# Performance work log

Hardware: AMD Instinct MI355X
Metric: run time of the kernel (lower is better)

Reference implementation:

```python
import jax, jax.numpy as jnp
import numpy as np

N_SRC0, N_DST0, N_DST1 = 100000, 25000, 5000
E0, E1 = 800000, 160000
D = 256


def setup_inputs() -> dict:
    key = jax.random.key(0)
    k = jax.random.split(key, 7)
    return {
        "x": jax.random.normal(k[0], (N_SRC0, D), dtype=jnp.float32),
        "ew0": jax.random.uniform(k[1], (E0,), dtype=jnp.float32),
        "ew1": jax.random.uniform(k[2], (E1,), dtype=jnp.float32),
        "src0": jax.random.randint(k[3], (E0,), 0, N_SRC0, dtype=jnp.int32),
        "dst0": jax.random.randint(k[4], (E0,), 0, N_DST0, dtype=jnp.int32),
        "src1": jax.random.randint(k[5], (E1,), 0, N_DST0, dtype=jnp.int32),
        "dst1": jax.random.randint(k[6], (E1,), 0, N_DST1, dtype=jnp.int32),
    }


def _block(x, src, dst, ew, n_dst):
    # u_mul_e + sum: gather src features, scale by edge weight, scatter-sum to dst
    msgs = x[src] * ew[:, None]            # [E, D]
    return jax.ops.segment_sum(msgs, dst, num_segments=n_dst)  # [n_dst, D]


def reference(x, ew0, ew1, src0, dst0, src1, dst1):
    h = _block(x, src0, dst0, ew0, N_DST0)   # block 0: [N_DST0, D]
    h = _block(h, src1, dst1, ew1, N_DST1)   # block 1: [N_DST1, D]
    return h
```

## Files before the change

### kernel.cpp

```cpp
#include <hip/hip_runtime.h>

constexpr int D       = 256;
constexpr int DV4     = D / 4;
constexpr int N_DST0  = 25000;
constexpr int N_DST1  = 5000;
constexpr int NARENA  = 8;
constexpr int CAPX    = 24;


__device__ __forceinline__ unsigned pack_bf16(float a, float b) {
    unsigned ua = __float_as_uint(a);
    unsigned ub = __float_as_uint(b);
    ua = (ua + 0x7FFFu + ((ua >> 16) & 1u)) >> 16;
    ub = (ub + 0x7FFFu + ((ub >> 16) & 1u)) >> 16;
    return ua | (ub << 16);
}

__device__ __forceinline__ void fma8_bf16(float* acc, uint4 v, float w) {
    acc[0] += __uint_as_float(v.x << 16)          * w;
    acc[1] += __uint_as_float(v.x & 0xFFFF0000u)  * w;
    acc[2] += __uint_as_float(v.y << 16)          * w;
    acc[3] += __uint_as_float(v.y & 0xFFFF0000u)  * w;
    acc[4] += __uint_as_float(v.z << 16)          * w;
    acc[5] += __uint_as_float(v.z & 0xFFFF0000u)  * w;
    acc[6] += __uint_as_float(v.w << 16)          * w;
    acc[7] += __uint_as_float(v.w & 0xFFFF0000u)  * w;
}

__device__ __forceinline__ unsigned pack_edge(int s, float w) {
    unsigned wq = (unsigned)(w * 32768.0f + 0.5f);
    wq = min(wq, 32767u);
    return (unsigned)s | (wq << 17);
}


__global__ __launch_bounds__(256) void prep_fused(
    const float4* __restrict__ x4, uint2* __restrict__ xb, int n4, int Gc,
    const int* __restrict__ src0, const float* __restrict__ ew0,
    const int* __restrict__ dst0, int E0, int* __restrict__ cnt0,
    unsigned* __restrict__ meta0,
    const int* __restrict__ src1, const float* __restrict__ ew1,
    const int* __restrict__ dst1, int E1, int* __restrict__ cnt1,
    unsigned* __restrict__ meta1)
{
    if (blockIdx.x < Gc) {
        int i = blockIdx.x * blockDim.x + threadIdx.x;
        int stride = Gc * blockDim.x;
        for (; i < n4; i += stride) {
            float4 v = x4[i];
            xb[i] = make_uint2(pack_bf16(v.x, v.y), pack_bf16(v.z, v.w));
        }
    } else {
        int arena = blockIdx.x & (NARENA - 1);
        int i = (blockIdx.x - Gc) * blockDim.x + threadIdx.x;
        int stride = (gridDim.x - Gc) * blockDim.x;
        int total = E0 + E1;
        for (; i < total; i += stride) {
            if (i < E0) {
                int s = src0[i];
                float w = ew0[i];
                int d = dst0[i];
                int p = atomicAdd(&cnt0[arena * N_DST0 + d], 1);
                if (p < CAPX)
                    meta0[((size_t)arena * N_DST0 + d) * CAPX + p] = pack_edge(s, w);
            } else {
                int q = i - E0;
                int s = src1[q];
                float w = ew1[q];
                int d = dst1[q];
                int p = atomicAdd(&cnt1[arena * N_DST1 + d], 1);
                if (p < CAPX)
                    meta1[((size_t)arena * N_DST1 + d) * CAPX + p] = pack_edge(s, w);
            }
        }
    }
}


template <bool OUT_BF16>
__global__ __launch_bounds__(256) void gather_cap(
    const uint4* __restrict__ xb4,
    const uint*  __restrict__ meta,
    const int*   __restrict__ cnt,
    void*        __restrict__ outp,
    int n_dst)
{
    int wave = (int)((blockIdx.x * blockDim.x + threadIdx.x) >> 6);
    int lane = threadIdx.x & 63;
    if (wave >= n_dst) return;

    int half = lane >> 5;
    int c16  = lane & 31;

    int cx = (lane < NARENA) ? min(cnt[lane * n_dst + wave], CAPX) : 0;
    int o[NARENA + 1];
    o[0] = 0;
    #pragma unroll
    for (int x = 0; x < NARENA; ++x) o[x + 1] = o[x] + __shfl(cx, x, 64);
    int n = o[NARENA];

    float acc[8] = {0.f,0.f,0.f,0.f,0.f,0.f,0.f,0.f};

    for (int base = 0; base < n; base += 64) {
        int i = base + lane;
        int2 mm = make_int2(0, 0);
        if (i < n) {
            int x = 0;
            #pragma unroll
            for (int y = 1; y < NARENA; ++y) if (i >= o[y]) x = y;
            unsigned u = meta[((size_t)x * n_dst + wave) * CAPX + (i - o[x])];
            mm.x = (int)(u & 0x1FFFFu);
            mm.y = __float_as_int((float)(u >> 17) * (1.0f / 32768.0f));
        }
        int nk = min(64, n - base);

        for (int e = 0; e < nk; e += 8) {
            int   sA = __shfl(mm.x, e + 0 + half, 64);
            int   sB = __shfl(mm.x, e + 2 + half, 64);
            int   sC = __shfl(mm.x, e + 4 + half, 64);
            int   sD = __shfl(mm.x, e + 6 + half, 64);
            float wA = __int_as_float(__shfl(mm.y, e + 0 + half, 64));
            float wB = __int_as_float(__shfl(mm.y, e + 2 + half, 64));
            float wC = __int_as_float(__shfl(mm.y, e + 4 + half, 64));
            float wD = __int_as_float(__shfl(mm.y, e + 6 + half, 64));
            uint4 vA = xb4[(size_t)sA * 32 + c16];
            uint4 vB = xb4[(size_t)sB * 32 + c16];
            uint4 vC = xb4[(size_t)sC * 32 + c16];
            uint4 vD = xb4[(size_t)sD * 32 + c16];
            fma8_bf16(acc, vA, wA);
            fma8_bf16(acc, vB, wB);
            fma8_bf16(acc, vC, wC);
            fma8_bf16(acc, vD, wD);
        }
    }

    #pragma unroll
    for (int j = 0; j < 8; ++j) acc[j] += __shfl_xor(acc[j], 32, 64);

    if (half == 0) {
        if (OUT_BF16) {
            uint4 o4;
            o4.x = pack_bf16(acc[0], acc[1]);
            o4.y = pack_bf16(acc[2], acc[3]);
            o4.z = pack_bf16(acc[4], acc[5]);
            o4.w = pack_bf16(acc[6], acc[7]);
            ((uint4*)outp)[(size_t)wave * 32 + c16] = o4;
        } else {
            float4* of = (float4*)outp;
            of[(size_t)wave * 64 + c16 * 2 + 0] = make_float4(acc[0], acc[1], acc[2], acc[3]);
            of[(size_t)wave * 64 + c16 * 2 + 1] = make_float4(acc[4], acc[5], acc[6], acc[7]);
        }
    }
}


__global__ __launch_bounds__(256) void hist_both(
    const int* __restrict__ dst0, int E0, int* __restrict__ cnt0,
    const int* __restrict__ dst1, int E1, int* __restrict__ cnt1)
{
    int i = blockIdx.x * blockDim.x + threadIdx.x;
    int stride = gridDim.x * blockDim.x;
    int total = E0 + E1;
    for (; i < total; i += stride) {
        if (i < E0) atomicAdd(&cnt0[dst0[i]], 1);
        else        atomicAdd(&cnt1[dst1[i - E0]], 1);
    }
}

__device__ void scan_one(int* cnt, int* row, int n)
{
    const int T = 1024;
    int t   = threadIdx.x;
    int per = (n + T - 1) / T;
    int b   = t * per;
    int e   = min(b + per, n);

    int local = 0;
    for (int i = b; i < e; ++i) local += cnt[i];

    int lane = t & 63, wid = t >> 6;
    int v = local;
    #pragma unroll
    for (int off = 1; off < 64; off <<= 1) {
        int u = __shfl_up(v, off, 64);
        if (lane >= off) v += u;
    }

    __shared__ int wsum[16], woff[16];
    if (lane == 63) wsum[wid] = v;
    __syncthreads();
    if (t == 0) {
        int run = 0;
        #pragma unroll
        for (int i = 0; i < 16; ++i) { woff[i] = run; run += wsum[i]; }
        row[n] = run;
    }
    __syncthreads();

    int run = woff[wid] + (v - local);
    for (int i = b; i < e; ++i) {
        int c = cnt[i];
        row[i] = run;
        cnt[i] = run;
        run += c;
    }
}

__global__ __launch_bounds__(1024) void scan_both(
    int* cnt0, int* row0, int n0, int* cnt1, int* row1, int n1)
{
    if (blockIdx.x == 0) scan_one(cnt0, row0, n0);
    else                 scan_one(cnt1, row1, n1);
}

__global__ __launch_bounds__(256) void scatter_both(
    const int* __restrict__ src0, const float* __restrict__ ew0,
    const int* __restrict__ dst0, int E0, int* __restrict__ cur0,
    int2* __restrict__ meta0,
    const int* __restrict__ src1, const float* __restrict__ ew1,
    const int* __restrict__ dst1, int E1, int* __restrict__ cur1,
    int2* __restrict__ meta1)
{
    int i = blockIdx.x * blockDim.x + threadIdx.x;
    int stride = gridDim.x * blockDim.x;
    int total = E0 + E1;
    for (; i < total; i += stride) {
        if (i < E0) {
            int p = atomicAdd(&cur0[dst0[i]], 1);
            meta0[p] = make_int2(src0[i], __float_as_int(ew0[i]));
        } else {
            int j = i - E0;
            int p = atomicAdd(&cur1[dst1[j]], 1);
            meta1[p] = make_int2(src1[j], __float_as_int(ew1[j]));
        }
    }
}

__global__ __launch_bounds__(256) void gather_rows_f32(
    const float* __restrict__ xin,
    const int2*  __restrict__ meta,
    const int*   __restrict__ row_start,
    float*       __restrict__ outp,
    int n_dst)
{
    int wave = (int)((blockIdx.x * blockDim.x + threadIdx.x) >> 6);
    int lane = threadIdx.x & 63;
    if (wave >= n_dst) return;

    int beg = row_start[wave];
    int end = row_start[wave + 1];
    const float4* xv = reinterpret_cast<const float4*>(xin);

    float4 acc = {0.f, 0.f, 0.f, 0.f};
    for (int base = beg; base < end; base += 64) {
        int idx = base + lane;
        int2 m = (idx < end) ? meta[idx] : make_int2(0, 0);
        int nk = min(64, end - base);
        int k = 0;
        for (; k + 4 <= nk; k += 4) {
            float4 v0 = xv[(size_t)__shfl(m.x, k + 0, 64) * DV4 + lane];
            float4 v1 = xv[(size_t)__shfl(m.x, k + 1, 64) * DV4 + lane];
            float4 v2 = xv[(size_t)__shfl(m.x, k + 2, 64) * DV4 + lane];
            float4 v3 = xv[(size_t)__shfl(m.x, k + 3, 64) * DV4 + lane];
            float w0 = __int_as_float(__shfl(m.y, k + 0, 64));
            float w1 = __int_as_float(__shfl(m.y, k + 1, 64));
            float w2 = __int_as_float(__shfl(m.y, k + 2, 64));
            float w3 = __int_as_float(__shfl(m.y, k + 3, 64));
            acc.x += v0.x * w0; acc.y += v0.y * w0; acc.z += v0.z * w0; acc.w += v0.w * w0;
            acc.x += v1.x * w1; acc.y += v1.y * w1; acc.z += v1.z * w1; acc.w += v1.w * w1;
            acc.x += v2.x * w2; acc.y += v2.y * w2; acc.z += v2.z * w2; acc.w += v2.w * w2;
            acc.x += v3.x * w3; acc.y += v3.y * w3; acc.z += v3.z * w3; acc.w += v3.w * w3;
        }
        for (; k < nk; ++k) {
            float4 v = xv[(size_t)__shfl(m.x, k, 64) * DV4 + lane];
            float w  = __int_as_float(__shfl(m.y, k, 64));
            acc.x += v.x * w; acc.y += v.y * w; acc.z += v.z * w; acc.w += v.w * w;
        }
    }
    reinterpret_cast<float4*>(outp)[(size_t)wave * DV4 + lane] = acc;
}


extern "C" void kernel_launch(void* const* d_in, const int* in_sizes, int n_in,
                              void* d_out, int out_size, void* d_ws, size_t ws_size,
                              hipStream_t stream) {
    const float* x    = (const float*)d_in[0];
    const float* ew0  = (const float*)d_in[1];
    const float* ew1  = (const float*)d_in[2];
    const int*   src0 = (const int*)d_in[3];
    const int*   dst0 = (const int*)d_in[4];
    const int*   src1 = (const int*)d_in[5];
    const int*   dst1 = (const int*)d_in[6];
    float*       out  = (float*)d_out;

    const int E0    = in_sizes[1];
    const int E1    = in_sizes[2];
    const int N_SRC = in_sizes[0] / D;

    const int blk = 256;
    int g0 = (N_DST0 * 64 + blk - 1) / blk;
    int g1 = (N_DST1 * 64 + blk - 1) / blk;
    int n4 = N_SRC * D / 4;

    size_t need_t1 =
        (size_t)N_SRC * D * 2 +
        (size_t)N_DST0 * D * 2 +
        (size_t)NARENA * N_DST0 * CAPX * 4 +
        (size_t)NARENA * N_DST1 * CAPX * 4 +
        (size_t)NARENA * (N_DST0 + N_DST1) * 4 +
        1024;

    if (ws_size >= need_t1) {
        char* p = (char*)d_ws;
        uint2* xb    = (uint2*)p;    p += (size_t)N_SRC * D * 2;
        uint2* h0b   = (uint2*)p;    p += (size_t)N_DST0 * D * 2;
        unsigned* meta0 = (unsigned*)p; p += (size_t)NARENA * N_DST0 * CAPX * 4;
        unsigned* meta1 = (unsigned*)p; p += (size_t)NARENA * N_DST1 * CAPX * 4;
        int*   cnt0  = (int*)p;      p += (size_t)NARENA * N_DST0 * 4;
        int*   cnt1  = (int*)p;      p += (size_t)NARENA * N_DST1 * 4;

        hipMemsetAsync(cnt0, 0, (size_t)NARENA * (N_DST0 + N_DST1) * 4, stream);

        const int Gc = 1024, Gs = 2048;
        prep_fused<<<Gc + Gs, blk, 0, stream>>>(
            (const float4*)x, xb, n4, Gc,
            src0, ew0, dst0, E0, cnt0, meta0,
            src1, ew1, dst1, E1, cnt1, meta1);

        gather_cap<true ><<<g0, blk, 0, stream>>>(
            (const uint4*)xb,  meta0, cnt0, (void*)h0b, N_DST0);
        gather_cap<false><<<g1, blk, 0, stream>>>(
            (const uint4*)h0b, meta1, cnt1, (void*)out, N_DST1);
    } else {
        char* p = (char*)d_ws;
        float* h0    = (float*)p; p += (size_t)N_DST0 * D * sizeof(float);
        int2*  meta0 = (int2*)p;  p += (size_t)E0 * sizeof(int2);
        int2*  meta1 = (int2*)p;  p += (size_t)E1 * sizeof(int2);
        int*   cnt0  = (int*)p;   p += (size_t)N_DST0 * sizeof(int);
        int*   row0  = (int*)p;   p += (size_t)(N_DST0 + 1) * sizeof(int);
        int*   cnt1  = (int*)p;   p += (size_t)N_DST1 * sizeof(int);
        int*   row1  = (int*)p;   p += (size_t)(N_DST1 + 1) * sizeof(int);

        hipMemsetAsync(cnt0, 0, (size_t)N_DST0 * sizeof(int), stream);
        hipMemsetAsync(cnt1, 0, (size_t)N_DST1 * sizeof(int), stream);

        int gEdges = min((E0 + E1 + blk - 1) / blk, 3840);
        hist_both<<<gEdges, blk, 0, stream>>>(dst0, E0, cnt0, dst1, E1, cnt1);
        scan_both<<<2, 1024, 0, stream>>>(cnt0, row0, N_DST0, cnt1, row1, N_DST1);
        scatter_both<<<gEdges, blk, 0, stream>>>(src0, ew0, dst0, E0, cnt0, meta0,
                                                 src1, ew1, dst1, E1, cnt1, meta1);
        gather_rows_f32<<<g0, blk, 0, stream>>>(x,  meta0, row0, h0,  N_DST0);
        gather_rows_f32<<<g1, blk, 0, stream>>>(h0, meta1, row1, out, N_DST1);
    }
}
```

Before: 140.5 us.

## Move block-1 edge scatter into block-0 gather kernel and rebalance prep grid

Block-1 edge bucketing no longer runs in the prep kernel. It now happens in dedicated blocks of the block-0 gather launch, so it overlaps with the block-0 gather. The prep kernel handles only the bf16 conversion and block-0 scatter, with its block split changed to 1280 convert and 768 scatter blocks. The fallback path's edge grid cap is also reduced. This shortens the critical prep phase, but the extra scatter blocks compete with the bandwidth-heavy gather for resources.

```diff
diff --git a/kernel.cpp b/kernel.cpp
--- a/kernel.cpp
+++ b/kernel.cpp
@@ -34,61 +34,31 @@
 }
 
 
-__global__ __launch_bounds__(256) void prep_fused(
-    const float4* __restrict__ x4, uint2* __restrict__ xb, int n4, int Gc,
-    const int* __restrict__ src0, const float* __restrict__ ew0,
-    const int* __restrict__ dst0, int E0, int* __restrict__ cnt0,
-    unsigned* __restrict__ meta0,
-    const int* __restrict__ src1, const float* __restrict__ ew1,
-    const int* __restrict__ dst1, int E1, int* __restrict__ cnt1,
-    unsigned* __restrict__ meta1)
-{
-    if (blockIdx.x < Gc) {
-        int i = blockIdx.x * blockDim.x + threadIdx.x;
-        int stride = Gc * blockDim.x;
-        for (; i < n4; i += stride) {
-            float4 v = x4[i];
-            xb[i] = make_uint2(pack_bf16(v.x, v.y), pack_bf16(v.z, v.w));
-        }
-    } else {
-        int arena = blockIdx.x & (NARENA - 1);
-        int i = (blockIdx.x - Gc) * blockDim.x + threadIdx.x;
-        int stride = (gridDim.x - Gc) * blockDim.x;
-        int total = E0 + E1;
-        for (; i < total; i += stride) {
-            if (i < E0) {
-                int s = src0[i];
-                float w = ew0[i];
-                int d = dst0[i];
-                int p = atomicAdd(&cnt0[arena * N_DST0 + d], 1);
-                if (p < CAPX)
-                    meta0[((size_t)arena * N_DST0 + d) * CAPX + p] = pack_edge(s, w);
-            } else {
-                int q = i - E0;
-                int s = src1[q];
-                float w = ew1[q];
-                int d = dst1[q];
-                int p = atomicAdd(&cnt1[arena * N_DST1 + d], 1);
-                if (p < CAPX)
-                    meta1[((size_t)arena * N_DST1 + d) * CAPX + p] = pack_edge(s, w);
-            }
-        }
+__device__ __forceinline__ void scatter_edges(
+    const int* __restrict__ src, const float* __restrict__ ew,
+    const int* __restrict__ dst, int E,
+    int* __restrict__ cnt, unsigned* __restrict__ meta, int n_dst,
+    int arena, int i0, int stride)
+{
+    for (int i = i0; i < E; i += stride) {
+        int s = src[i];
+        float w = ew[i];
+        int d = dst[i];
+        int p = atomicAdd(&cnt[arena * n_dst + d], 1);
+        if (p < CAPX)
+            meta[((size_t)arena * n_dst + d) * CAPX + p] = pack_edge(s, w);
     }
 }
 
 
 template <bool OUT_BF16>
-__global__ __launch_bounds__(256) void gather_cap(
+__device__ __forceinline__ void gather_row(
     const uint4* __restrict__ xb4,
-    const uint*  __restrict__ meta,
-    const int*   __restrict__ cnt,
-    void*        __restrict__ outp,
-    int n_dst)
-{
-    int wave = (int)((blockIdx.x * blockDim.x + threadIdx.x) >> 6);
-    int lane = threadIdx.x & 63;
-    if (wave >= n_dst) return;
-
+    const unsigned* __restrict__ meta,
+    const int* __restrict__ cnt,
+    void* __restrict__ outp,
+    int n_dst, int wave, int lane)
+{
     int half = lane >> 5;
     int c16  = lane & 31;
 
@@ -151,6 +121,62 @@
             of[(size_t)wave * 64 + c16 * 2 + 1] = make_float4(acc[4], acc[5], acc[6], acc[7]);
         }
     }
+}
+
+
+__global__ __launch_bounds__(256) void prep0(
+    const float4* __restrict__ x4, uint2* __restrict__ xb, int n4, int Gc,
+    const int* __restrict__ src0, const float* __restrict__ ew0,
+    const int* __restrict__ dst0, int E0,
+    int* __restrict__ cnt0, unsigned* __restrict__ meta0)
+{
+    if (blockIdx.x < Gc) {
+        int i = blockIdx.x * blockDim.x + threadIdx.x;
+        int stride = Gc * blockDim.x;
+        for (; i < n4; i += stride) {
+            float4 v = x4[i];
+            xb[i] = make_uint2(pack_bf16(v.x, v.y), pack_bf16(v.z, v.w));
+        }
+    } else {
+        int arena = blockIdx.x & (NARENA - 1);
+        int i0 = (blockIdx.x - Gc) * blockDim.x + threadIdx.x;
+        int stride = (gridDim.x - Gc) * blockDim.x;
+        scatter_edges(src0, ew0, dst0, E0, cnt0, meta0, N_DST0, arena, i0, stride);
+    }
+}
+
+
+__global__ __launch_bounds__(256) void gather0_scatter1(
+    const uint4* __restrict__ xb4,
+    const unsigned* __restrict__ meta0, const int* __restrict__ cnt0,
+    uint2* __restrict__ h0b,
+    const int* __restrict__ src1, const float* __restrict__ ew1,
+    const int* __restrict__ dst1, int E1,
+    int* __restrict__ cnt1, unsigned* __restrict__ meta1, int S1B)
+{
+    if ((int)blockIdx.x < S1B) {
+        int arena = blockIdx.x & (NARENA - 1);
+        int i0 = blockIdx.x * blockDim.x + threadIdx.x;
+        int stride = S1B * blockDim.x;
+        scatter_edges(src1, ew1, dst1, E1, cnt1, meta1, N_DST1, arena, i0, stride);
+        return;
+    }
+    int wave = (int)((((int)blockIdx.x - S1B) * blockDim.x + threadIdx.x) >> 6);
+    int lane = threadIdx.x & 63;
+    if (wave < N_DST0)
+        gather_row<true>(xb4, meta0, cnt0, (void*)h0b, N_DST0, wave, lane);
+}
+
+
+__global__ __launch_bounds__(256) void gather1_k(
+    const uint4* __restrict__ h0b4,
+    const unsigned* __restrict__ meta1, const int* __restrict__ cnt1,
+    float* __restrict__ outp)
+{
+    int wave = (int)((blockIdx.x * blockDim.x + threadIdx.x) >> 6);
+    int lane = threadIdx.x & 63;
+    if (wave < N_DST1)
+        gather_row<false>(h0b4, meta1, cnt1, (void*)outp, N_DST1, wave, lane);
 }
 
 
@@ -298,8 +324,6 @@
     const int N_SRC = in_sizes[0] / D;
 
     const int blk = 256;
-    int g0 = (N_DST0 * 64 + blk - 1) / blk;
-    int g1 = (N_DST1 * 64 + blk - 1) / blk;
     int n4 = N_SRC * D / 4;
 
     size_t need_t1 =
@@ -321,16 +345,20 @@
 
         hipMemsetAsync(cnt0, 0, (size_t)NARENA * (N_DST0 + N_DST1) * 4, stream);
 
-        const int Gc = 1024, Gs = 2048;
-        prep_fused<<<Gc + Gs, blk, 0, stream>>>(
+        const int Gc = 1280, Gs = 768;
+        prep0<<<Gc + Gs, blk, 0, stream>>>(
             (const float4*)x, xb, n4, Gc,
-            src0, ew0, dst0, E0, cnt0, meta0,
-            src1, ew1, dst1, E1, cnt1, meta1);
-
-        gather_cap<true ><<<g0, blk, 0, stream>>>(
-            (const uint4*)xb,  meta0, cnt0, (void*)h0b, N_DST0);
-        gather_cap<false><<<g1, blk, 0, stream>>>(
-            (const uint4*)h0b, meta1, cnt1, (void*)out, N_DST1);
+            src0, ew0, dst0, E0, cnt0, meta0);
+
+        const int S1B = 512;
+        int g0 = S1B + (N_DST0 * 64 + blk - 1) / blk;
+        gather0_scatter1<<<g0, blk, 0, stream>>>(
+            (const uint4*)xb, meta0, cnt0, h0b,
+            src1, ew1, dst1, E1, cnt1, meta1, S1B);
+
+        int g1 = (N_DST1 * 64 + blk - 1) / blk;
+        gather1_k<<<g1, blk, 0, stream>>>(
+            (const uint4*)h0b, meta1, cnt1, out);
     } else {
         char* p = (char*)d_ws;
         float* h0    = (float*)p; p += (size_t)N_DST0 * D * sizeof(float);
@@ -344,11 +372,13 @@
         hipMemsetAsync(cnt0, 0, (size_t)N_DST0 * sizeof(int), stream);
         hipMemsetAsync(cnt1, 0, (size_t)N_DST1 * sizeof(int), stream);
 
-        int gEdges = min((E0 + E1 + blk - 1) / blk, 3840);
+        int gEdges = min((E0 + E1 + blk - 1) / blk, 2048);
         hist_both<<<gEdges, blk, 0, stream>>>(dst0, E0, cnt0, dst1, E1, cnt1);
         scan_both<<<2, 1024, 0, stream>>>(cnt0, row0, N_DST0, cnt1, row1, N_DST1);
         scatter_both<<<gEdges, blk, 0, stream>>>(src0, ew0, dst0, E0, cnt0, meta0,
                                                  src1, ew1, dst1, E1, cnt1, meta1);
+        int g0 = (N_DST0 * 64 + blk - 1) / blk;
+        int g1 = (N_DST1 * 64 + blk - 1) / blk;
         gather_rows_f32<<<g0, blk, 0, stream>>>(x,  meta0, row0, h0,  N_DST0);
         gather_rows_f32<<<g1, blk, 0, stream>>>(h0, meta1, row1, out, N_DST1);
     }
```

Measured after the change: 133.0 us. -5.3%, faster.
